# Kernel tuning notes

Hardware: AMD Instinct MI355X
Metric: run time of the kernel (lower is better)

## Reference

```python
import jax, jax.numpy as jnp
import numpy as np

D_MODEL = 256
N_HEAD = 4
N_LAYERS = 2
D_FF = 4 * D_MODEL
VOCAB = 4096
DINO = 384
T_SEQ = 40
N_PATCH = 256
B = 32
LN_EPS = 1e-5


def setup_inputs() -> dict:
    key = jax.random.key(0)
    ks = jax.random.split(key, 24)
    f = jnp.float32
    d = {}
    d['patches'] = jax.random.normal(ks[0], (B, N_PATCH, DINO), dtype=f)
    d['tokens'] = jax.random.randint(ks[1], (B, T_SEQ), 0, VOCAB)
    s = 0.02
    d['embedding'] = jax.random.normal(ks[2], (VOCAB, D_MODEL), dtype=f) * s
    d['pos_emb'] = jax.random.normal(ks[3], (T_SEQ, D_MODEL), dtype=f) * s
    d['in_proj_w'] = jax.random.normal(ks[4], (N_LAYERS, 3 * D_MODEL, D_MODEL), dtype=f) * s
    d['in_proj_b'] = jnp.zeros((N_LAYERS, 3 * D_MODEL), dtype=f)
    d['out_proj_w'] = jax.random.normal(ks[5], (N_LAYERS, D_MODEL, D_MODEL), dtype=f) * s
    d['out_proj_b'] = jnp.zeros((N_LAYERS, D_MODEL), dtype=f)
    d['lin1_w'] = jax.random.normal(ks[6], (N_LAYERS, D_FF, D_MODEL), dtype=f) * s
    d['lin1_b'] = jnp.zeros((N_LAYERS, D_FF), dtype=f)
    d['lin2_w'] = jax.random.normal(ks[7], (N_LAYERS, D_MODEL, D_FF), dtype=f) * s
    d['lin2_b'] = jnp.zeros((N_LAYERS, D_MODEL), dtype=f)
    d['ln1_g'] = jnp.ones((N_LAYERS, D_MODEL), dtype=f)
    d['ln1_b'] = jnp.zeros((N_LAYERS, D_MODEL), dtype=f)
    d['ln2_g'] = jnp.ones((N_LAYERS, D_MODEL), dtype=f)
    d['ln2_b'] = jnp.zeros((N_LAYERS, D_MODEL), dtype=f)
    d['fus_w1'] = jax.random.normal(ks[8], (D_MODEL, DINO + D_MODEL), dtype=f) * s
    d['fus_b1'] = jnp.zeros((D_MODEL,), dtype=f)
    d['fus_w2'] = jax.random.normal(ks[9], (D_MODEL, D_MODEL), dtype=f) * s
    d['fus_b2'] = jnp.zeros((D_MODEL,), dtype=f)
    d['cls_w'] = jax.random.normal(ks[10], (VOCAB, D_MODEL), dtype=f) * s
    d['cls_b'] = jnp.zeros((VOCAB,), dtype=f)
    return d


def _layer_norm(x, g, b):
    m = jnp.mean(x, axis=-1, keepdims=True)
    v = jnp.mean((x - m) ** 2, axis=-1, keepdims=True)
    return (x - m) / jnp.sqrt(v + LN_EPS) * g + b


def _encode(x, mask, in_proj_w, in_proj_b, out_proj_w, out_proj_b,
            lin1_w, lin1_b, lin2_w, lin2_b, ln1_g, ln1_b, ln2_g, ln2_b):
    # x: [N, S, d], mask: [N, S] bool (True = valid key). Post-norm encoder, relu FFN.
    N, S, d = x.shape
    hd = d // N_HEAD
    for i in range(N_LAYERS):
        qkv = x @ in_proj_w[i].T + in_proj_b[i]
        q, k, v = jnp.split(qkv, 3, axis=-1)
        sh = lambda t: t.reshape(N, S, N_HEAD, hd).transpose(0, 2, 1, 3)
        q, k, v = sh(q), sh(k), sh(v)
        sc = jnp.einsum('nhqd,nhkd->nhqk', q, k) / np.sqrt(hd)
        sc = jnp.where(mask[:, None, None, :], sc, -1e9)
        a = jax.nn.softmax(sc, axis=-1)
        o = jnp.einsum('nhqk,nhkd->nhqd', a, v).transpose(0, 2, 1, 3).reshape(N, S, d)
        o = o @ out_proj_w[i].T + out_proj_b[i]
        x = _layer_norm(x + o, ln1_g[i], ln1_b[i])
        ff = jax.nn.relu(x @ lin1_w[i].T + lin1_b[i]) @ lin2_w[i].T + lin2_b[i]
        x = _layer_norm(x + ff, ln2_g[i], ln2_b[i])
    return x


def reference(patches, tokens, embedding, pos_emb, in_proj_w, in_proj_b,
              out_proj_w, out_proj_b, lin1_w, lin1_b, lin2_w, lin2_b,
              ln1_g, ln1_b, ln2_g, ln2_b, fus_w1, fus_b1, fus_w2, fus_b2,
              cls_w, cls_b):
    Bsz, T = tokens.shape
    d = embedding.shape[1]
    emb = embedding[tokens] + pos_emb[None, :T, :]      # [B, T, d]
    Tm1 = T - 1
    # All 39 prefix runs at once: prefix of length t+1 == full seq with keys > t masked.
    X = jnp.broadcast_to(emb[None], (Tm1, Bsz, T, d)).reshape(Tm1 * Bsz, T, d)
    valid = jnp.arange(T)[None, :] <= jnp.arange(Tm1)[:, None]  # [Tm1, T]
    mask = jnp.broadcast_to(valid[:, None, :], (Tm1, Bsz, T)).reshape(Tm1 * Bsz, T)
    enc = _encode(X, mask, in_proj_w, in_proj_b, out_proj_w, out_proj_b,
                  lin1_w, lin1_b, lin2_w, lin2_b, ln1_g, ln1_b, ln2_g, ln2_b)
    enc = enc.reshape(Tm1, Bsz, T, d)
    idx = jnp.arange(Tm1)
    ctx_rest = enc[idx, :, idx, :]                      # [Tm1, B, d] last valid position
    ctx = jnp.concatenate([jnp.zeros((1, Bsz, d), emb.dtype), ctx_rest], axis=0)  # [T, B, d]
    # Fusion MLP: split first linear into patch part (t-invariant) + context part.
    w1p, w1c = fus_w1[:, :DINO], fus_w1[:, DINO:]
    pp = jnp.einsum('bpd,kd->bpk', patches, w1p)        # [B, P, d]
    cp = jnp.einsum('tbd,kd->tbk', ctx, w1c) + fus_b1   # [T, B, d]
    h = jax.nn.gelu(pp[None] + cp[:, :, None, :], approximate=False)  # [T, B, P, d]
    feat = jnp.einsum('tbpk,mk->tbpm', h, fus_w2) + fus_b2            # [T, B, P, d]
    # Gather-only classification: prob of tokens[:, t] at step t.
    targets = tokens.T                                   # [T, B]
    cw = cls_w[targets]                                  # [T, B, d]
    cb = cls_b[targets]                                  # [T, B]
    logits = jnp.einsum('tbpm,tbm->tbp', feat, cw) + cb[:, :, None]
    probs = jax.nn.sigmoid(logits)                       # [T, B, P]
    return probs.transpose(1, 2, 0)                      # [B, P, T]
```

## Files before the change

kernel.cpp:

```cpp
#include <hip/hip_runtime.h>
#include <math.h>

#define DM    256
#define NH    4
#define HD    64
#define TS    40
#define TM1   39
#define BB    32
#define DFF   1024
#define DINO  384
#define NPATCH 256
#define VOCAB 4096

#define NTOK  24960
#define NQ2   1248

typedef _Float16 f16;
typedef __attribute__((ext_vector_type(8))) _Float16 half8;
typedef __attribute__((ext_vector_type(4))) _Float16 half4;
typedef __attribute__((ext_vector_type(4))) float f32x4;

#define OFF_EMBH   0u
#define OFF_EMB    163840u
#define OFF_QKVH   491520u
#define OFF_X1     983040u
#define OFF_X1H    7372800u
#define OFF_H1     10567680u
#define OFF_BIG    16957440u
#define   BT_AO1H  6389760u
#define   BT_X2    6553600u
#define   BT_X2H   6881280u
#define   BT_FF2H  7045120u
#define   BT_H1H   7700480u
#define OFF_CTX    29736960u
#define OFF_CPB    30064640u
#define OFF_U      30392320u
#define OFF_S      30720000u
#define OFF_WQKVH  30722048u
#define OFF_WQ1H   30820352u
#define OFF_KVWH   30853120u
#define OFF_WOH    30918656u
#define OFF_WOH1   30951424u
#define OFF_L1WH   30984192u
#define OFF_L1WH1  31115264u
#define OFF_L2WH   31246336u
#define OFF_L2WH1  31377408u
#define OFF_W1PH   31508480u
#define OFF_W1CH   31557632u
#define OFF_FW2TH  31590400u
#define OFF_CWGH   31623168u
#define OFF_MAP    31787008u
#define WS_FLOATS  31813216u

__global__ __launch_bounds__(256) void prep_kernel(
    const int* __restrict__ tokens, const float* __restrict__ etab,
    const float* __restrict__ pos,
    const float* __restrict__ ipw, const float* __restrict__ opw,
    const float* __restrict__ l1w, const float* __restrict__ l2w,
    const float* __restrict__ fw1, const float* __restrict__ fw2,
    const float* __restrict__ clsw, const float* __restrict__ clsb,
    const float* __restrict__ fb2,
    float* __restrict__ emb, f16* __restrict__ embh,
    f16* __restrict__ wqkvh, f16* __restrict__ wq1h, f16* __restrict__ kvwh,
    f16* __restrict__ woh, f16* __restrict__ woh1,
    f16* __restrict__ l1wh, f16* __restrict__ l1wh1,
    f16* __restrict__ l2wh, f16* __restrict__ l2wh1,
    f16* __restrict__ w1ph, f16* __restrict__ w1ch, f16* __restrict__ fw2th,
    f16* __restrict__ cwgh, float* __restrict__ sv, float* __restrict__ ctx,
    int* __restrict__ map1, int* __restrict__ map2)
{
    int i = blockIdx.x * 256 + threadIdx.x;
    if (i < 327680) {
        int r = i >> 8, j = i & 255;
        int p = r % TS;
        float v = etab[(size_t)tokens[r] * DM + j] + pos[p * DM + j];
        emb[i] = v; embh[i] = (f16)v;
        return;
    }
    i -= 327680;
    if (i < 196608) { wqkvh[i] = (f16)ipw[i]; return; }
    i -= 196608;
    if (i < 65536)  { wq1h[i] = (f16)ipw[196608 + i]; return; }
    i -= 65536;
    if (i < 131072) { kvwh[i] = (f16)ipw[262144 + i]; return; }
    i -= 131072;
    if (i < 65536)  { woh[i]  = (f16)opw[i]; return; }
    i -= 65536;
    if (i < 65536)  { woh1[i] = (f16)opw[65536 + i]; return; }
    i -= 65536;
    if (i < 262144) { l1wh[i]  = (f16)l1w[i]; return; }
    i -= 262144;
    if (i < 262144) { l1wh1[i] = (f16)l1w[262144 + i]; return; }
    i -= 262144;
    if (i < 262144) { l2wh[i]  = (f16)l2w[i]; return; }
    i -= 262144;
    if (i < 262144) { l2wh1[i] = (f16)l2w[262144 + i]; return; }
    i -= 262144;
    if (i < 98304) {
        int r = i / 384, c = i - r * 384;
        w1ph[i] = (f16)fw1[r * 640 + c];
        return;
    }
    i -= 98304;
    if (i < 65536) {
        int n = i >> 8, k = i & 255;
        w1ch[i] = (f16)fw1[n * 640 + 384 + k];
        return;
    }
    i -= 65536;
    if (i < 65536) {
        int j = i >> 8, k = i & 255;
        fw2th[i] = (f16)fw2[k * 256 + j];
        return;
    }
    i -= 65536;
    if (i < 327680) {
        int tb = i >> 8, j = i & 255;
        int t = tb >> 5, b = tb & 31;
        cwgh[i] = (f16)clsw[(size_t)tokens[b * TS + t] * DM + j];
        return;
    }
    i -= 327680;
    if (i < 81920) {
        int tb = i >> 6, l = i & 63;
        int t = tb >> 5, b = tb & 31;
        int tok = tokens[b * TS + t];
        float a = 0.f;
#pragma unroll
        for (int c = 0; c < 4; ++c)
            a += fb2[l + 64 * c] * clsw[(size_t)tok * DM + l + 64 * c];
#pragma unroll
        for (int o = 32; o; o >>= 1) a += __shfl_xor(a, o);
        if (l == 0) sv[tb] = a + clsb[tok];
        return;
    }
    i -= 81920;
    if (i < 8192) { ctx[i] = 0.f; return; }
    i -= 8192;
    if (i < NQ2) {
        int t = i >> 5, b = i & 31;
        map2[i] = ((t * (t + 1)) / 2 + t) * 32 + b;
    }
    if (i < NTOK) {
        int q = i >> 5, b = i & 31;
        int t = 0;
        while (((t + 1) * (t + 2)) / 2 <= q) ++t;
        int p = q - (t * (t + 1)) / 2;
        map1[i] = b * TS + p;
    }
}

__device__ __forceinline__ void stage16(const f16* g, f16* lbase_wave_uniform) {
    __builtin_amdgcn_global_load_lds(
        (const __attribute__((address_space(1))) void*)g,
        (__attribute__((address_space(3))) void*)lbase_wave_uniform, 16, 0, 0);
}

__device__ __forceinline__ half8 load_frag8(const float* p) {
    float4 a0 = *(const float4*)p;
    float4 a1 = *(const float4*)(p + 4);
    half8 h;
    h[0] = (f16)a0.x; h[1] = (f16)a0.y; h[2] = (f16)a0.z; h[3] = (f16)a0.w;
    h[4] = (f16)a1.x; h[5] = (f16)a1.y; h[6] = (f16)a1.z; h[7] = (f16)a1.w;
    return h;
}

template <int BM, typename TA, bool RELU, bool OUTF16>
__global__ __launch_bounds__(256) void gemm_x(
    const TA* __restrict__ A, int lda,
    const f16* __restrict__ B, int ldb,
    const float* __restrict__ bias,
    void* __restrict__ Cv, int ldc, int K)
{
    constexpr int AF  = BM / 8;
    constexpr int TF  = AF + 16;
    constexpr int MRE = BM / 32;
    __shared__ __align__(16) f16 lds[TF * 512];
    int tid = threadIdx.x;
    int w = tid >> 6, l = tid & 63;
    int m0 = blockIdx.y * BM, n0 = blockIdx.x << 7;
    int lrow = l & 15;
    int lk8  = (l >> 4) << 3;
    int wm = w >> 1, wn = w & 1;

    f32x4 acc[MRE][4] = {};

    for (int k0 = 0; k0 < K; k0 += 64) {
#pragma unroll
        for (int j = 0; j < TF / 4; ++j) {
            int f = (j << 2) | w;
            if (f < AF) {
                int mi = f >> 1, kc = f & 1;
                const TA* ga = A + (size_t)(m0 + (mi << 4) + lrow) * lda + k0 + (kc << 5) + lk8;
                if constexpr (__is_same(TA, f16)) {
                    stage16(ga, &lds[f << 9]);
                } else {
                    *(half8*)&lds[(f << 9) + (l << 3)] = load_frag8(ga);
                }
            } else {
                int fb = f - AF;
                int nj = fb >> 1, kc = fb & 1;
                const f16* gb = B + (size_t)(n0 + (nj << 4) + lrow) * ldb + k0 + (kc << 5) + lk8;
                stage16(gb, &lds[f << 9]);
            }
        }
        __syncthreads();
#pragma unroll
        for (int kc = 0; kc < 2; ++kc) {
            half8 af[MRE], bfr[4];
#pragma unroll
            for (int i = 0; i < MRE; ++i)
                af[i] = *(half8*)&lds[((((wm * MRE + i) << 1) | kc) << 9) + (l << 3)];
#pragma unroll
            for (int j2 = 0; j2 < 4; ++j2)
                bfr[j2] = *(half8*)&lds[((AF + ((((wn << 2) | j2) << 1) | kc)) << 9) + (l << 3)];
#pragma unroll
            for (int i = 0; i < MRE; ++i)
#pragma unroll
                for (int j2 = 0; j2 < 4; ++j2)
                    acc[i][j2] = __builtin_amdgcn_mfma_f32_16x16x32_f16(
                        af[i], bfr[j2], acc[i][j2], 0, 0, 0);
        }
        __syncthreads();
    }

    int colq = l & 15, rowq = (l >> 4) << 2;
#pragma unroll
    for (int i = 0; i < MRE; ++i) {
        int gmb = m0 + (wm * MRE + i) * 16 + rowq;
#pragma unroll
        for (int j2 = 0; j2 < 4; ++j2) {
            int gn = n0 + ((wn << 2) | j2) * 16 + colq;
            float bv = bias ? bias[gn] : 0.f;
#pragma unroll
            for (int r = 0; r < 4; ++r) {
                float v = acc[i][j2][r] + bv;
                if (RELU) v = fmaxf(v, 0.f);
                if (OUTF16)
                    ((f16*)Cv)[(size_t)(gmb + r) * ldc + gn] = (f16)v;
                else
                    ((float*)Cv)[(size_t)(gmb + r) * ldc + gn] = v;
            }
        }
    }
}

__global__ __launch_bounds__(256) void ln_kernel(
    float* __restrict__ X, const float* __restrict__ res,
    const int* __restrict__ map, const float* __restrict__ g,
    const float* __restrict__ beta, int nrows, f16* __restrict__ outh)
{
    int r = blockIdx.x * 4 + (threadIdx.x >> 6);
    if (r >= nrows) return;
    int l = threadIdx.x & 63;
    float* xp = X + (size_t)r * DM + l * 4;
    float4 v = *(float4*)xp;
    if (res) {
        int rr = map ? map[r] : r;
        float4 rv = *(const float4*)(res + (size_t)rr * DM + l * 4);
        v.x += rv.x; v.y += rv.y; v.z += rv.z; v.w += rv.w;
    }
    float s = v.x + v.y + v.z + v.w;
#pragma unroll
    for (int o = 32; o; o >>= 1) s += __shfl_xor(s, o);
    float mean = s * (1.f / 256.f);
    float dx = v.x - mean, dy = v.y - mean, dz = v.z - mean, dw = v.w - mean;
    float s2 = dx * dx + dy * dy + dz * dz + dw * dw;
#pragma unroll
    for (int o = 32; o; o >>= 1) s2 += __shfl_xor(s2, o);
    float rstd = 1.f / sqrtf(s2 * (1.f / 256.f) + 1e-5f);
    float4 gv = *(const float4*)(g + l * 4);
    float4 bv = *(const float4*)(beta + l * 4);
    float4 ov;
    ov.x = dx * rstd * gv.x + bv.x;
    ov.y = dy * rstd * gv.y + bv.y;
    ov.z = dz * rstd * gv.z + bv.z;
    ov.w = dw * rstd * gv.w + bv.w;
    *(float4*)xp = ov;
    if (outh) {
        half4 oh;
        oh[0] = (f16)ov.x; oh[1] = (f16)ov.y; oh[2] = (f16)ov.z; oh[3] = (f16)ov.w;
        *(half4*)(outh + (size_t)r * DM + l * 4) = oh;
    }
}

__global__ __launch_bounds__(256) void attn0_kernel(
    const f16* __restrict__ qkv, f16* __restrict__ ao)
{
    int bp = blockIdx.x;
    int b = bp / 39, p = bp % 39;
    int tid = threadIdx.x;
    int h = tid >> 6, l = tid & 63;

    float qv = (float)qkv[(size_t)(b * TS + p) * 768 + h * 64 + l];

    int krow = (l < 39) ? l : 38;
    const f16* Kr = qkv + (size_t)(b * TS + krow) * 768 + 256 + h * 64;
    float acc = 0.f;
#pragma unroll
    for (int c = 0; c < 8; ++c) {
        half8 k8 = *(const half8*)(Kr + c * 8);
#pragma unroll
        for (int j = 0; j < 8; ++j)
            acc += __shfl(qv, c * 8 + j) * (float)k8[j];
    }
    float s = acc * 0.125f;

    float m = -1e30f, lsum = 0.f, o = 0.f;
    for (int t = p; t < TM1; ++t) {
        float st = __shfl(s, t);
        float mnew = fmaxf(m, st);
        float c = __expf(m - mnew);
        float e = __expf(st - mnew);
        lsum = lsum * c + e;
        float vv = (float)qkv[(size_t)(b * TS + t) * 768 + 512 + h * 64 + l];
        o = o * c + e * vv;
        m = mnew;
        int row = ((t * (t + 1)) >> 1) + p;
        ao[((size_t)row * 32 + b) * DM + h * 64 + l] = (f16)(o / lsum);
    }
}

__global__ __launch_bounds__(256) void attn1_kernel(
    const float* __restrict__ h1, const f16* __restrict__ kv1,
    const f16* __restrict__ Wq, const float* __restrict__ bq,
    f16* __restrict__ ao1)
{
    int tb = blockIdx.x;
    int t = tb >> 5, b = tb & 31;
    int tid = threadIdx.x;
    int h = tid >> 6, l = tid & 63;
    int tri = (t * (t + 1)) >> 1;
    __shared__ float h1r[DM];
    h1r[tid] = h1[((size_t)(tri + t) * 32 + b) * DM + tid];
    __syncthreads();

    float q = bq[h * 64 + l];
    const half8* w8 = (const half8*)(Wq + (size_t)(h * 64 + l) * DM);
#pragma unroll 8
    for (int c = 0; c < 32; ++c) {
        half8 ww = w8[c];
#pragma unroll
        for (int j = 0; j < 8; ++j)
            q += (float)ww[j] * h1r[c * 8 + j];
    }

    int kr = (l <= t) ? l : t;
    const f16* Kp = kv1 + ((size_t)(tri + kr) * 32 + b) * 512 + h * 64;
    float sc = 0.f;
#pragma unroll
    for (int c = 0; c < 8; ++c) {
        half8 k8 = *(const half8*)(Kp + c * 8);
#pragma unroll
        for (int j = 0; j < 8; ++j)
            sc += __shfl(q, c * 8 + j) * (float)k8[j];
    }
    sc = (l <= t) ? sc * 0.125f : -1e30f;
    float m = sc;
#pragma unroll
    for (int o = 32; o; o >>= 1) m = fmaxf(m, __shfl_xor(m, o));
    float e = (l <= t) ? __expf(sc - m) : 0.f;
    float ss = e;
#pragma unroll
    for (int o = 32; o; o >>= 1) ss += __shfl_xor(ss, o);
    float a = e / ss;

    float o = 0.f;
    for (int k = 0; k <= t; ++k) {
        float ak = __shfl(a, k);
        o += ak * (float)kv1[((size_t)(tri + k) * 32 + b) * 512 + 256 + h * 64 + l];
    }
    ao1[(size_t)tb * DM + h * 64 + l] = (f16)o;
}

__device__ __forceinline__ float gelu_f(float x)
{
    float ax = fabsf(x);
    float z  = ax * 0.70710678118654752440f;
    float d  = 1.f + z * (0.278393f + z * (0.230389f + z * (0.000972f + z * 0.078108f)));
    float d2 = d * d;
    float E  = 1.f - __builtin_amdgcn_rcpf(d2 * d2);
    return 0.5f * x + 0.5f * ax * E;
}

__global__ __launch_bounds__(256) void final_out(
    const f16* __restrict__ pp, const float* __restrict__ cpb,
    const float* __restrict__ u, const float* __restrict__ sv,
    float* __restrict__ out)
{
    int bp = blockIdx.x;
    int b = bp >> 8;
    int tid = threadIdx.x;
    int w = tid >> 6, l = tid & 63;
    const f16* ppr = pp + (size_t)bp * DM + l * 4;
    float p0 = (float)ppr[0], p1 = (float)ppr[1];
    float p2 = (float)ppr[2], p3 = (float)ppr[3];
    for (int t = w; t < TS; t += 4) {
        int tb = t * 32 + b;
        float4 cp = *(const float4*)(cpb + (size_t)tb * DM + l * 4);
        float4 uu = *(const float4*)(u + (size_t)tb * DM + l * 4);
        float v = gelu_f(p0 + cp.x) * uu.x + gelu_f(p1 + cp.y) * uu.y +
                  gelu_f(p2 + cp.z) * uu.z + gelu_f(p3 + cp.w) * uu.w;
#pragma unroll
        for (int off = 32; off; off >>= 1) v += __shfl_xor(v, off);
        if (l == 0) out[(size_t)bp * TS + t] = 1.f / (1.f + __expf(-(v + sv[tb])));
    }
}

extern "C" void kernel_launch(void* const* d_in, const int* in_sizes, int n_in,
                              void* d_out, int out_size, void* d_ws, size_t ws_size,
                              hipStream_t stream)
{
    (void)in_sizes; (void)n_in; (void)out_size;
    const float* patches   = (const float*)d_in[0];
    const int*   tokens    = (const int*)  d_in[1];
    const float* embedding = (const float*)d_in[2];
    const float* pos_emb   = (const float*)d_in[3];
    const float* in_proj_w = (const float*)d_in[4];
    const float* in_proj_b = (const float*)d_in[5];
    const float* out_proj_w= (const float*)d_in[6];
    const float* out_proj_b= (const float*)d_in[7];
    const float* lin1_w    = (const float*)d_in[8];
    const float* lin1_b    = (const float*)d_in[9];
    const float* lin2_w    = (const float*)d_in[10];
    const float* lin2_b    = (const float*)d_in[11];
    const float* ln1_g     = (const float*)d_in[12];
    const float* ln1_b     = (const float*)d_in[13];
    const float* ln2_g     = (const float*)d_in[14];
    const float* ln2_b     = (const float*)d_in[15];
    const float* fus_w1    = (const float*)d_in[16];
    const float* fus_b1    = (const float*)d_in[17];
    const float* fus_w2    = (const float*)d_in[18];
    const float* fus_b2    = (const float*)d_in[19];
    const float* cls_w     = (const float*)d_in[20];
    const float* cls_b     = (const float*)d_in[21];

    if (ws_size < (size_t)WS_FLOATS * 4) return;

    float* ws   = (float*)d_ws;
    f16*   embh = (f16*)(ws + OFF_EMBH);
    float* emb  = ws + OFF_EMB;
    f16*   qkvh = (f16*)(ws + OFF_QKVH);
    float* x1   = ws + OFF_X1;
    f16*   x1h  = (f16*)(ws + OFF_X1H);
    f16*   pph  = (f16*)(ws + OFF_X1H);
    float* h1   = ws + OFF_H1;
    float* big  = ws + OFF_BIG;
    f16*   ao0h = (f16*)big;
    f16*   ff1h = (f16*)big;
    f16*   kv1h = (f16*)big;
    f16*   ao1h = (f16*)(big + BT_AO1H);
    float* x2   = big + BT_X2;
    f16*   x2h  = (f16*)(big + BT_X2H);
    f16*   ff2h = (f16*)(big + BT_FF2H);
    f16*   h1h  = (f16*)(big + BT_H1H);
    float* ctx  = ws + OFF_CTX;
    float* cpb  = ws + OFF_CPB;
    float* u    = ws + OFF_U;
    float* svec = ws + OFF_S;
    f16*   wqkvh= (f16*)(ws + OFF_WQKVH);
    f16*   wq1h = (f16*)(ws + OFF_WQ1H);
    f16*   kvwh = (f16*)(ws + OFF_KVWH);
    f16*   woh  = (f16*)(ws + OFF_WOH);
    f16*   woh1 = (f16*)(ws + OFF_WOH1);
    f16*   l1wh = (f16*)(ws + OFF_L1WH);
    f16*   l1wh1= (f16*)(ws + OFF_L1WH1);
    f16*   l2wh = (f16*)(ws + OFF_L2WH);
    f16*   l2wh1= (f16*)(ws + OFF_L2WH1);
    f16*   w1ph = (f16*)(ws + OFF_W1PH);
    f16*   w1ch = (f16*)(ws + OFF_W1CH);
    f16*   fw2th= (f16*)(ws + OFF_FW2TH);
    f16*   cwgh = (f16*)(ws + OFF_CWGH);
    int*   map1 = (int*)(ws + OFF_MAP);
    int*   map2 = map1 + NTOK;

    prep_kernel<<<10050, 256, 0, stream>>>(
        tokens, embedding, pos_emb, in_proj_w, out_proj_w, lin1_w, lin2_w,
        fus_w1, fus_w2, cls_w, cls_b, fus_b2,
        emb, embh, wqkvh, wq1h, kvwh, woh, woh1, l1wh, l1wh1, l2wh, l2wh1,
        w1ph, w1ch, fw2th, cwgh, svec, ctx, map1, map2);

    gemm_x<64, f16, false, false><<<dim3(2, 20), 256, 0, stream>>>(
        cwgh, DM, fw2th, DM, nullptr, u, DM, DM);

    gemm_x<64, f16, false, true><<<dim3(6, 20), 256, 0, stream>>>(
        embh, DM, wqkvh, DM, in_proj_b, qkvh, 768, DM);
    attn0_kernel<<<NQ2, 256, 0, stream>>>(qkvh, ao0h);
    gemm_x<64, f16, false, false><<<dim3(2, 390), 256, 0, stream>>>(
        ao0h, DM, woh, DM, out_proj_b, x1, DM, DM);
    ln_kernel<<<6240, 256, 0, stream>>>(x1, emb, map1, ln1_g, ln1_b, NTOK, x1h);
    gemm_x<128, f16, true, true><<<dim3(8, 195), 256, 0, stream>>>(
        x1h, DM, l1wh, DM, lin1_b, ff1h, DFF, DM);
    gemm_x<64, f16, false, false><<<dim3(2, 390), 256, 0, stream>>>(
        ff1h, DFF, l2wh, DFF, lin2_b, h1, DM, DFF);
    ln_kernel<<<6240, 256, 0, stream>>>(h1, x1, nullptr, ln2_g, ln2_b, NTOK, h1h);

    gemm_x<64, float, false, true><<<dim3(2, 128), 256, 0, stream>>>(
        patches, DINO, w1ph, DINO, nullptr, pph, DM, DINO);

    gemm_x<128, f16, false, true><<<dim3(4, 195), 256, 0, stream>>>(
        h1h, DM, kvwh, DM, in_proj_b + 768 + 256, kv1h, 512, DM);
    attn1_kernel<<<NQ2, 256, 0, stream>>>(
        h1, kv1h, wq1h, in_proj_b + 768, ao1h);
    gemm_x<64, f16, false, false><<<dim3(2, 20), 256, 0, stream>>>(
        ao1h, DM, woh1, DM, out_proj_b + DM, x2, DM, DM);
    ln_kernel<<<312, 256, 0, stream>>>(x2, h1, map2, ln1_g + DM, ln1_b + DM, NQ2, x2h);
    gemm_x<64, f16, true, true><<<dim3(8, 20), 256, 0, stream>>>(
        x2h, DM, l1wh1, DM, lin1_b + DFF, ff2h, DFF, DM);
    gemm_x<64, f16, false, false><<<dim3(2, 20), 256, 0, stream>>>(
        ff2h, DFF, l2wh1, DFF, lin2_b + DM, ctx + BB * DM, DM, DFF);
    ln_kernel<<<312, 256, 0, stream>>>(ctx + BB * DM, x2, nullptr, ln2_g + DM, ln2_b + DM, NQ2, nullptr);

    gemm_x<64, float, false, false><<<dim3(2, 20), 256, 0, stream>>>(
        ctx, DM, w1ch, DM, fus_b1, cpb, DM, DM);

    final_out<<<BB * NPATCH, 256, 0, stream>>>(pph, cpb, u, svec, (float*)d_out);
}
```

Before: 465.4 us.

## Double-buffer LDS staging in f16 GEMM to overlap async loads with MFMA

For GEMMs whose A operand is already f16, the kernel now allocates two LDS buffers and issues the asynchronous global-to-LDS copy for the next K tile before computing on the current one. Partial vmcnt waits with raw barriers replace the full __syncthreads pair, so load latency can hide behind MFMA work. LDS use doubles, which may lower occupancy. Correctness depends on stage16 issuing exactly LPW vmem ops per wave. The fp32-A path is unchanged.

After: 447.1 us. 3.9% less time.

```diff
diff --git a/kernel.cpp b/kernel.cpp
--- a/kernel.cpp
+++ b/kernel.cpp
@@ -175,7 +175,10 @@
     constexpr int AF  = BM / 8;
     constexpr int TF  = AF + 16;
     constexpr int MRE = BM / 32;
-    __shared__ __align__(16) f16 lds[TF * 512];
+    constexpr int LPW = TF / 4;
+    constexpr bool ASYNC = __is_same(TA, f16);
+    constexpr int NBUF = ASYNC ? 2 : 1;
+    __shared__ __align__(16) f16 lds[NBUF * TF * 512];
     int tid = threadIdx.x;
     int w = tid >> 6, l = tid & 63;
     int m0 = blockIdx.y * BM, n0 = blockIdx.x << 7;
@@ -185,35 +188,37 @@
 
     f32x4 acc[MRE][4] = {};
 
-    for (int k0 = 0; k0 < K; k0 += 64) {
+    auto stage = [&](f16* dst, int k0) {
 #pragma unroll
         for (int j = 0; j < TF / 4; ++j) {
             int f = (j << 2) | w;
             if (f < AF) {
                 int mi = f >> 1, kc = f & 1;
                 const TA* ga = A + (size_t)(m0 + (mi << 4) + lrow) * lda + k0 + (kc << 5) + lk8;
-                if constexpr (__is_same(TA, f16)) {
-                    stage16(ga, &lds[f << 9]);
+                if constexpr (ASYNC) {
+                    stage16((const f16*)ga, dst + (f << 9));
                 } else {
-                    *(half8*)&lds[(f << 9) + (l << 3)] = load_frag8(ga);
+                    *(half8*)&dst[(f << 9) + (l << 3)] = load_frag8((const float*)ga);
                 }
             } else {
                 int fb = f - AF;
                 int nj = fb >> 1, kc = fb & 1;
                 const f16* gb = B + (size_t)(n0 + (nj << 4) + lrow) * ldb + k0 + (kc << 5) + lk8;
-                stage16(gb, &lds[f << 9]);
+                stage16(gb, dst + (f << 9));
             }
         }
-        __syncthreads();
+    };
+
+    auto compute = [&](const f16* buf) {
 #pragma unroll
         for (int kc = 0; kc < 2; ++kc) {
             half8 af[MRE], bfr[4];
 #pragma unroll
             for (int i = 0; i < MRE; ++i)
-                af[i] = *(half8*)&lds[((((wm * MRE + i) << 1) | kc) << 9) + (l << 3)];
+                af[i] = *(const half8*)&buf[((((wm * MRE + i) << 1) | kc) << 9) + (l << 3)];
 #pragma unroll
             for (int j2 = 0; j2 < 4; ++j2)
-                bfr[j2] = *(half8*)&lds[((AF + ((((wn << 2) | j2) << 1) | kc)) << 9) + (l << 3)];
+                bfr[j2] = *(const half8*)&buf[((AF + ((((wn << 2) | j2) << 1) | kc)) << 9) + (l << 3)];
 #pragma unroll
             for (int i = 0; i < MRE; ++i)
 #pragma unroll
@@ -221,7 +226,33 @@
                     acc[i][j2] = __builtin_amdgcn_mfma_f32_16x16x32_f16(
                         af[i], bfr[j2], acc[i][j2], 0, 0, 0);
         }
-        __syncthreads();
+    };
+
+    if constexpr (ASYNC) {
+        int nk = K >> 6;
+        stage(lds, 0);
+        for (int t = 0; t < nk; ++t) {
+            f16* cur = lds + (t & 1) * (TF * 512);
+            if (t + 1 < nk) {
+                stage(lds + ((t + 1) & 1) * (TF * 512), (t + 1) << 6);
+                asm volatile("s_waitcnt vmcnt(%0)" :: "i"(LPW) : "memory");
+            } else {
+                asm volatile("s_waitcnt vmcnt(0)" ::: "memory");
+            }
+            __builtin_amdgcn_s_barrier();
+            asm volatile("" ::: "memory");
+            compute(cur);
+            asm volatile("" ::: "memory");
+            __builtin_amdgcn_s_barrier();
+            asm volatile("" ::: "memory");
+        }
+    } else {
+        for (int k0 = 0; k0 < K; k0 += 64) {
+            stage(lds, k0);
+            __syncthreads();
+            compute(lds);
+            __syncthreads();
+        }
     }
 
     int colq = l & 15, rowq = (l >> 4) << 2;
```
